# Kernel tuning notes

Hardware: AMD Instinct MI355X
Metric: run time of the kernel (lower is better)

The kernel has to match this reference:

```python
import jax, jax.numpy as jnp
import numpy as np

GAMMA = -0.1   # l0_gamma
ZETA = 1.1     # l0_zeta
BETA = 0.66    # l0_beta (hard-concrete temperature)
LAMBDA = 0.01  # lambda_reg (post-warmup current_lambda)
EPS = 1e-12


def _layernorm(x, g, b, eps=1e-5):
    mu = jnp.mean(x, axis=-1, keepdims=True)
    var = jnp.var(x, axis=-1, keepdims=True)
    return (x - mu) / jnp.sqrt(var + eps) * g + b


def setup_inputs() -> dict:
    key = jax.random.key(0)
    ks = jax.random.split(key, 12)
    B, N, D, H, E, C = 8, 512, 512, 256, 32, 2
    node_feat = jax.random.normal(ks[0], (B, N, D), jnp.float32)
    labels = jax.random.randint(ks[1], (B,), 0, C)
    a = (jax.random.uniform(ks[2], (B, N, N)) < 0.05).astype(jnp.float32)
    adjs = jnp.maximum(a, jnp.swapaxes(a, 1, 2)) * (1.0 - jnp.eye(N, dtype=jnp.float32))
    masks = jnp.ones((B, N), jnp.float32)
    init = lambda k, shp, fan: jax.random.normal(k, shp, jnp.float32) / np.sqrt(fan).astype(np.float32)
    return {
        "node_feat": node_feat, "labels": labels, "adjs": adjs, "masks": masks,
        # edge scorer MLP: concat([h_i,h_j]) -> edge_dim -> 1, factorized as Wa@h_i + Wb@h_j
        "Wa": init(ks[3], (D, E), D), "Wb": init(ks[4], (D, E), D), "be": jnp.zeros((E,), jnp.float32),
        "W2e": init(ks[5], (E, 1), E), "b2e": jnp.zeros((1,), jnp.float32),
        # conv: Linear(feature_dim, hidden_dim)
        "Wconv": init(ks[6], (D, H), D), "bconv": jnp.zeros((H,), jnp.float32),
        # classifier: Linear(H,H//2) -> ReLU -> LayerNorm -> spectral_norm(Linear(H//2,C))
        "W1c": init(ks[7], (H, H // 2), H), "b1c": jnp.zeros((H // 2,), jnp.float32),
        "ln_g": jnp.ones((H // 2,), jnp.float32), "ln_b": jnp.zeros((H // 2,), jnp.float32),
        "W2c": init(ks[8], (H // 2, C), H // 2), "b2c": jnp.zeros((C,), jnp.float32),
        "u_sn": jax.random.normal(ks[9], (C,), jnp.float32),  # spectral-norm power-iteration buffer
    }


def reference(node_feat, labels, adjs, masks, Wa, Wb, be, W2e, b2e,
              Wconv, bconv, W1c, b1c, ln_g, ln_b, W2c, b2c, u_sn):
    B = node_feat.shape[0]
    # F.normalize(node_feat, p=2, dim=2)
    nrm = jnp.sqrt(jnp.sum(node_feat * node_feat, axis=2, keepdims=True))
    nf = node_feat / jnp.maximum(nrm, EPS)
    # edge scoring: logAlpha[b,i,j] = MLP([h_i ; h_j])
    e1 = nf @ Wa                                  # [B,N,E]
    e2 = nf @ Wb                                  # [B,N,E]
    hpair = jax.nn.relu(e1[:, :, None, :] + e2[:, None, :, :] + be)   # [B,N,N,E]
    logAlpha = jnp.einsum('bije,e->bij', hpair, W2e[:, 0]) + b2e[0]    # [B,N,N]
    # deterministic hard-concrete gate (eval mode): clip(sigmoid(logAlpha)*(zeta-gamma)+gamma, 0, 1)
    gate = jnp.clip(jax.nn.sigmoid(logAlpha) * (ZETA - GAMMA) + GAMMA, 0.0, 1.0)
    edge_weights = gate * adjs
    # aggregate: row-normalized weighted adjacency
    wadj = adjs * edge_weights
    row_sum = jnp.sum(wadj, axis=2, keepdims=True) + 1e-8
    h = jnp.einsum('bij,bjd->bid', wadj / row_sum, nf)
    h = jax.nn.relu(h @ Wconv + bconv)            # [B,N,H]
    # edge-weighted attention pooling: node importance = weighted degree, masked softmax
    imp = jnp.sum(wadj, axis=2)                    # [B,N]
    attn_logits = jnp.where(masks > 0, imp, -1e9)
    attn = jax.nn.softmax(attn_logits, axis=1)
    graph_rep = jnp.einsum('bn,bnh->bh', attn, h)  # [B,H]
    # classifier
    z = jax.nn.relu(graph_rep @ W1c + b1c)
    z = _layernorm(z, ln_g, ln_b)
    # spectral norm (1 power iteration, u/v stop-gradded like torch buffers)
    v = W2c @ u_sn
    v = jax.lax.stop_gradient(v / jnp.maximum(jnp.linalg.norm(v), EPS))
    u2 = W2c.T @ v
    u2 = jax.lax.stop_gradient(u2 / jnp.maximum(jnp.linalg.norm(u2), EPS))
    sigma = v @ (W2c @ u2)
    logits = z @ (W2c / sigma) + b2c              # [B,C]
    # losses
    logp = jax.nn.log_softmax(logits, axis=1)
    cls_loss = -jnp.mean(logp[jnp.arange(B), labels])
    l0_penalty = jnp.sum(jax.nn.sigmoid(logAlpha - BETA * jnp.log(-GAMMA / ZETA)))
    total_loss = cls_loss + LAMBDA * l0_penalty
    return logits, total_loss, adjs * edge_weights
```

## Files before the change

### kernel.cpp

```cpp
#include <hip/hip_runtime.h>


#define Bsz 8
#define Nn  512
#define Dd  512
#define Hh  256
#define Ee  32

#define WS_NFCPK  0L
#define WS_E1     524288L
#define WS_E2     655360L
#define WS_WADJB  786432L
#define WS_RS     1835008L
#define WS_L0     1839104L
#define WS_GR     1839112L
#define WS_WABPK  1841160L
#define WS_WCPK   1857544L

typedef __bf16 bf16x8 __attribute__((ext_vector_type(8)));
typedef float  f32x4  __attribute__((ext_vector_type(4)));

__device__ inline ushort f2bf(float f) {
  union { float f; unsigned u; } c; c.f = f;
  return (ushort)((c.u + 0x7fffu + ((c.u >> 16) & 1u)) >> 16);
}

__global__ __launch_bounds__(256) void pack_weights(
    const float* __restrict__ Wconv, const float* __restrict__ Wa,
    const float* __restrict__ Wb, ushort* __restrict__ wcpk,
    ushort* __restrict__ wabpk)
{
  const int g = blockIdx.x*256 + threadIdx.x;
  if (g < 16384) {
    const int kq = g >> 8, n = g & 255;
    ushort tmp[8];
    #pragma unroll
    for (int j = 0; j < 8; ++j) tmp[j] = f2bf(Wconv[(kq*8 + j)*Hh + n]);
    *(uint4*)(wcpk + (long)g*8) = *(uint4*)tmp;
  } else if (g < 16384 + 4096) {
    const int gg = g - 16384;
    const int kq = gg >> 6, n = gg & 63;
    const float* W = (n < 32) ? Wa : Wb;
    const int e = n & 31;
    ushort tmp[8];
    #pragma unroll
    for (int j = 0; j < 8; ++j) tmp[j] = f2bf(W[(kq*8 + j)*Ee + e]);
    *(uint4*)(wabpk + (long)gg*8) = *(uint4*)tmp;
  }
}

__global__ __launch_bounds__(256) void norm_e12_nfc(
    const float* __restrict__ nfeat, const ushort* __restrict__ wabpk,
    const ushort* __restrict__ wcpk, const float* __restrict__ be,
    ushort* __restrict__ nfcpk, float* __restrict__ e1, float* __restrict__ e2,
    float* __restrict__ row_sum, float* __restrict__ gr,
    float* __restrict__ l0_sum)
{
  const int blk = blockIdx.x;
  const int r0 = blk*16;
  const int b = r0 >> 9;
  const int t = threadIdx.x;
  const int r = t >> 4;
  const int seg = t & 15;

  __shared__ ushort As[(63*17 + 15 + 1)*8];
  __shared__ ushort BsA[2][4*64*8];
  __shared__ ushort BsC[2][4*256*8];

  float4 v[8];
  const float* src = nfeat + (long)(r0 + r)*Dd + seg*32;
  #pragma unroll
  for (int i = 0; i < 8; ++i) v[i] = *(const float4*)(src + i*4);
  float s = 0.f;
  #pragma unroll
  for (int i = 0; i < 8; ++i)
    s += v[i].x*v[i].x + v[i].y*v[i].y + v[i].z*v[i].z + v[i].w*v[i].w;
  #pragma unroll
  for (int m = 1; m < 16; m <<= 1) s += __shfl_xor(s, m, 16);
  const float sc = 1.f / fmaxf(sqrtf(s), 1e-12f);
  #pragma unroll
  for (int q = 0; q < 4; ++q) {
    ushort tmp[8];
    const float4 a = v[2*q], bq = v[2*q+1];
    tmp[0]=f2bf(a.x*sc);  tmp[1]=f2bf(a.y*sc);  tmp[2]=f2bf(a.z*sc);  tmp[3]=f2bf(a.w*sc);
    tmp[4]=f2bf(bq.x*sc); tmp[5]=f2bf(bq.y*sc); tmp[6]=f2bf(bq.z*sc); tmp[7]=f2bf(bq.w*sc);
    *(uint4*)(As + ((seg*4 + q)*17 + r)*8) = *(uint4*)tmp;
  }
  if (t < 16) row_sum[r0 + t] = 0.f;
  if (blk == 0) {
    for (int p = t; p < Bsz*Hh; p += 256) gr[p] = 0.f;
    if (t == 0) *l0_sum = 0.f;
  }

  const int lane = t & 63, l15 = lane & 15, quad = lane >> 4;
  const int w = t >> 6;
  const int abq = t >> 6, abn = t & 63;

  f32x4 acc_e = {0.f, 0.f, 0.f, 0.f};
  f32x4 acc_c[4];
  #pragma unroll
  for (int j = 0; j < 4; ++j) acc_c[j] = (f32x4){0.f,0.f,0.f,0.f};

  uint4 pab = *(const uint4*)(wabpk + ((long)abq*64 + abn)*8);
  uint4 pc[4];
  #pragma unroll
  for (int p = 0; p < 4; ++p) {
    const int g = t + p*256;
    pc[p] = *(const uint4*)(wcpk + ((long)(g >> 8)*256 + (g & 255))*8);
  }
  *(uint4*)(BsA[0] + (abq*64 + abn)*8) = pab;
  #pragma unroll
  for (int p = 0; p < 4; ++p) {
    const int g = t + p*256;
    *(uint4*)(BsC[0] + ((g >> 8)*256 + (g & 255))*8) = pc[p];
  }
  {
    pab = *(const uint4*)(wabpk + ((long)(4 + abq)*64 + abn)*8);
    #pragma unroll
    for (int p = 0; p < 4; ++p) {
      const int g = t + p*256;
      pc[p] = *(const uint4*)(wcpk + ((long)(4 + (g >> 8))*256 + (g & 255))*8);
    }
  }

  for (int k0 = 0; k0 < 512; k0 += 32) {
    const int pb = (k0 >> 5) & 1;
    __syncthreads();
    if (k0 + 32 < 512) {
      *(uint4*)(BsA[1-pb] + (abq*64 + abn)*8) = pab;
      #pragma unroll
      for (int p = 0; p < 4; ++p) {
        const int g = t + p*256;
        *(uint4*)(BsC[1-pb] + ((g >> 8)*256 + (g & 255))*8) = pc[p];
      }
      if (k0 + 64 < 512) {
        const int kb = (k0 + 64) >> 3;
        pab = *(const uint4*)(wabpk + ((long)(kb + abq)*64 + abn)*8);
        #pragma unroll
        for (int p = 0; p < 4; ++p) {
          const int g = t + p*256;
          pc[p] = *(const uint4*)(wcpk + ((long)(kb + (g >> 8))*256 + (g & 255))*8);
        }
      }
    }
    const bf16x8 af = *(const bf16x8*)(As + (((k0 >> 3) + quad)*17 + l15)*8);
    const bf16x8 bfa = *(const bf16x8*)(BsA[pb] + (quad*64 + w*16 + l15)*8);
    acc_e = __builtin_amdgcn_mfma_f32_16x16x32_bf16(af, bfa, acc_e, 0, 0, 0);
    #pragma unroll
    for (int fn = 0; fn < 4; ++fn) {
      const bf16x8 bfc = *(const bf16x8*)(BsC[pb] + (quad*256 + w*64 + fn*16 + l15)*8);
      acc_c[fn] = __builtin_amdgcn_mfma_f32_16x16x32_bf16(af, bfc, acc_c[fn], 0, 0, 0);
    }
  }

  {
    const int col = w*16 + l15;
    #pragma unroll
    for (int rr = 0; rr < 4; ++rr) {
      const int row = r0 + quad*4 + rr;
      if (col < 32) e1[(long)row*Ee + col] = acc_e[rr] + be[col];
      else          e2[(long)row*Ee + (col - 32)] = acc_e[rr];
    }
  }

  __syncthreads();
  ushort* tile = BsC[0];
  #pragma unroll
  for (int fn = 0; fn < 4; ++fn) {
    const int col = w*64 + fn*16 + l15;
    #pragma unroll
    for (int rr = 0; rr < 4; ++rr)
      tile[(quad*4 + rr)*260 + col] = f2bf(acc_c[fn][rr]);
  }
  __syncthreads();
  #pragma unroll
  for (int p = 0; p < 2; ++p) {
    const int g = t + p*256;
    const int oct = g >> 8, c = g & 255;
    ushort tmp[8];
    #pragma unroll
    for (int j = 0; j < 8; ++j) tmp[j] = tile[(oct*8 + j)*260 + c];
    const long og = ((r0 & 511) >> 3) + oct;
    *(uint4*)(nfcpk + ((long)b*16384 + og*256 + c)*8) = *(uint4*)tmp;
  }
}

__global__ __launch_bounds__(256) void edge_kernel(
    const float* __restrict__ e1, const float* __restrict__ e2,
    const float* __restrict__ W2e, const float* __restrict__ b2e,
    const float* __restrict__ adjs, float* __restrict__ out_wadj,
    ushort* __restrict__ wadj_b, float* __restrict__ row_sum,
    float* __restrict__ l0_sum)
{
  const int b  = blockIdx.z;
  const int i0 = blockIdx.y * 32;
  const int j0 = blockIdx.x * 128;
  const int t  = threadIdx.x;

  __shared__ float e2s[32*132];

  #pragma unroll
  for (int itr = 0; itr < 4; ++itr) {
    const int idx = t + itr*256;
    const int kq = idx & 7, jg = idx >> 3;
    const float4 v = *(const float4*)(e2 + ((long)(b*Nn + j0 + jg))*Ee + kq*4);
    e2s[(kq*4+0)*132 + jg] = v.x;
    e2s[(kq*4+1)*132 + jg] = v.y;
    e2s[(kq*4+2)*132 + jg] = v.z;
    e2s[(kq*4+3)*132 + jg] = v.w;
  }

  const int pair  = t >> 4;
  const int jslot = t & 15;
  const int ia = i0 + pair*2;
  const int ib = ia + 1;
  const int ja = jslot*4;
  const int jb = ja + 64;

  float e1af[32], e1bf[32], w2f[32];
  #pragma unroll
  for (int q = 0; q < 8; ++q) {
    *(float4*)(&e1af[q*4]) = *(const float4*)(e1 + ((long)(b*Nn + ia))*Ee + q*4);
    *(float4*)(&e1bf[q*4]) = *(const float4*)(e1 + ((long)(b*Nn + ib))*Ee + q*4);
    *(float4*)(&w2f[q*4])  = *(const float4*)(W2e + q*4);
  }
  const float b2 = b2e[0];
  __syncthreads();

  float acc[2][8] = {};
  #pragma unroll
  for (int k = 0; k < 32; ++k) {
    const float4 va = *(const float4*)(e2s + k*132 + ja);
    const float4 vb = *(const float4*)(e2s + k*132 + jb);
    const float w = w2f[k];
    const float ea = e1af[k], eb = e1bf[k];
    acc[0][0] += fmaxf(ea+va.x, 0.f)*w;
    acc[0][1] += fmaxf(ea+va.y, 0.f)*w;
    acc[0][2] += fmaxf(ea+va.z, 0.f)*w;
    acc[0][3] += fmaxf(ea+va.w, 0.f)*w;
    acc[0][4] += fmaxf(ea+vb.x, 0.f)*w;
    acc[0][5] += fmaxf(ea+vb.y, 0.f)*w;
    acc[0][6] += fmaxf(ea+vb.z, 0.f)*w;
    acc[0][7] += fmaxf(ea+vb.w, 0.f)*w;
    acc[1][0] += fmaxf(eb+va.x, 0.f)*w;
    acc[1][1] += fmaxf(eb+va.y, 0.f)*w;
    acc[1][2] += fmaxf(eb+va.z, 0.f)*w;
    acc[1][3] += fmaxf(eb+va.w, 0.f)*w;
    acc[1][4] += fmaxf(eb+vb.x, 0.f)*w;
    acc[1][5] += fmaxf(eb+vb.y, 0.f)*w;
    acc[1][6] += fmaxf(eb+vb.z, 0.f)*w;
    acc[1][7] += fmaxf(eb+vb.w, 0.f)*w;
  }

  float rs[2] = {0.f, 0.f};
  float l0acc = 0.f;
  #pragma unroll
  for (int ii = 0; ii < 2; ++ii) {
    const int i = (ii == 0) ? ia : ib;
    const float* arow = adjs     + ((long)(b*Nn + i))*Nn + j0;
    ushort* bwrow     = wadj_b   + ((long)(b*Nn + i))*Nn + j0;
    float* outrow     = out_wadj + ((long)(b*Nn + i))*Nn + j0;
    #pragma unroll
    for (int h2 = 0; h2 < 2; ++h2) {
      const int jl = (h2 == 0) ? ja : jb;
      const float4 av = *(const float4*)(arow + jl);
      float wv[4];
      #pragma unroll
      for (int c = 0; c < 4; ++c) {
        const float logA = acc[ii][h2*4 + c] + b2;
        const float e = expf(-logA);
        const float sg = 1.f/(1.f + e);
        const float gate = fminf(fmaxf(sg*1.2f - 0.1f, 0.f), 1.f);
        const float a = (c==0)?av.x:(c==1)?av.y:(c==2)?av.z:av.w;
        const float w = gate*a*a;
        wv[c] = w;
        rs[ii] += w;
        l0acc += 1.f/(1.f + 0.20543832f*e);
      }
      ushort4 bw;
      bw.x = f2bf(wv[0]); bw.y = f2bf(wv[1]); bw.z = f2bf(wv[2]); bw.w = f2bf(wv[3]);
      *(ushort4*)(bwrow + jl) = bw;
      outrow[jl+0] = wv[0]; outrow[jl+1] = wv[1];
      outrow[jl+2] = wv[2]; outrow[jl+3] = wv[3];
    }
  }

  #pragma unroll
  for (int m = 1; m < 16; m <<= 1) {
    rs[0] += __shfl_xor(rs[0], m, 16);
    rs[1] += __shfl_xor(rs[1], m, 16);
  }
  if (jslot == 0) {
    atomicAdd(&row_sum[b*Nn + ia], rs[0]);
    atomicAdd(&row_sum[b*Nn + ib], rs[1]);
  }
  #pragma unroll
  for (int m = 1; m < 64; m <<= 1) l0acc += __shfl_xor(l0acc, m, 64);
  if ((t & 63) == 0) atomicAdd(l0_sum, l0acc);
}

__global__ __launch_bounds__(256) void gemm_pool(
    const ushort* __restrict__ wadjb, const ushort* __restrict__ nfcpk,
    const float* __restrict__ row_sum, const float* __restrict__ masks,
    const float* __restrict__ bconv, float* __restrict__ gr)
{
  const int bb = blockIdx.z;
  const int m0 = blockIdx.y*64, n0 = blockIdx.x*64;
  const int t = threadIdx.x;
  const int lane = t & 63, l15 = lane & 15, quad = lane >> 4;
  const int wv = t >> 6, wr = wv & 1, wc = wv >> 1;

  __shared__ ushort As[2][259*8];
  __shared__ ushort Bs[2][256*8];
  __shared__ float ptile[64*65];
  __shared__ float red[8];
  __shared__ float attn_s[64];

  const ushort* Ab = wadjb + (long)bb*262144;
  const ushort* Bb = nfcpk + (long)bb*131072;
  const int am = t >> 2, akq = t & 3;
  const int bn = t & 63, bkq = t >> 6;

  f32x4 acc[2][2];
  #pragma unroll
  for (int i = 0; i < 2; ++i)
    #pragma unroll
    for (int j = 0; j < 2; ++j) acc[i][j] = (f32x4){0.f,0.f,0.f,0.f};

  uint4 ra = *(const uint4*)(Ab + (long)(m0+am)*512 + akq*8);
  uint4 rb = *(const uint4*)(Bb + ((long)bkq*256 + n0 + bn)*8);
  *(uint4*)(As[0] + (akq*65 + am)*8) = ra;
  *(uint4*)(Bs[0] + (bkq*64 + bn)*8) = rb;
  ra = *(const uint4*)(Ab + (long)(m0+am)*512 + 32 + akq*8);
  rb = *(const uint4*)(Bb + ((long)(4 + bkq)*256 + n0 + bn)*8);

  for (int k0 = 0; k0 < 512; k0 += 32) {
    const int pb = (k0 >> 5) & 1;
    __syncthreads();
    if (k0 + 32 < 512) {
      *(uint4*)(As[1-pb] + (akq*65 + am)*8) = ra;
      *(uint4*)(Bs[1-pb] + (bkq*64 + bn)*8) = rb;
      if (k0 + 64 < 512) {
        ra = *(const uint4*)(Ab + (long)(m0+am)*512 + (k0+64) + akq*8);
        rb = *(const uint4*)(Bb + ((long)(((k0+64) >> 3) + bkq)*256 + n0 + bn)*8);
      }
    }
    bf16x8 af[2], bfr[2];
    #pragma unroll
    for (int i = 0; i < 2; ++i)
      af[i] = *(const bf16x8*)(As[pb] + (quad*65 + wr*32 + i*16 + l15)*8);
    #pragma unroll
    for (int j = 0; j < 2; ++j)
      bfr[j] = *(const bf16x8*)(Bs[pb] + (quad*64 + wc*32 + j*16 + l15)*8);
    #pragma unroll
    for (int i = 0; i < 2; ++i)
      #pragma unroll
      for (int j = 0; j < 2; ++j)
        acc[i][j] = __builtin_amdgcn_mfma_f32_16x16x32_bf16(
            af[i], bfr[j], acc[i][j], 0, 0, 0);
  }
  __syncthreads();

  {
    const float mk0 = masks[bb*Nn + t], mk1 = masks[bb*Nn + t + 256];
    const float lv0 = (mk0 > 0.f) ? row_sum[bb*Nn + t] : -1e9f;
    const float lv1 = (mk1 > 0.f) ? row_sum[bb*Nn + t + 256] : -1e9f;
    float m = fmaxf(lv0, lv1);
    #pragma unroll
    for (int s = 1; s < 64; s <<= 1) m = fmaxf(m, __shfl_xor(m, s, 64));
    if (lane == 0) red[wv] = m;
    __syncthreads();
    const float mx = fmaxf(fmaxf(red[0], red[1]), fmaxf(red[2], red[3]));
    float sm = expf(lv0 - mx) + expf(lv1 - mx);
    #pragma unroll
    for (int s = 1; s < 64; s <<= 1) sm += __shfl_xor(sm, s, 64);
    if (lane == 0) red[4 + wv] = sm;
    __syncthreads();
    const float sinv = 1.f/(red[4] + red[5] + red[6] + red[7]);
    if (t < 64) {
      const int node = m0 + t;
      const float mm = masks[bb*Nn + node];
      const float lv = (mm > 0.f) ? row_sum[bb*Nn + node] : -1e9f;
      attn_s[t] = expf(lv - mx)*sinv;
    }
    __syncthreads();
  }

  #pragma unroll
  for (int i = 0; i < 2; ++i) {
    #pragma unroll
    for (int j = 0; j < 2; ++j) {
      const int lcol = wc*32 + j*16 + l15;
      const float bias = bconv[n0 + lcol];
      #pragma unroll
      for (int rr = 0; rr < 4; ++rr) {
        const int lrow = wr*32 + i*16 + quad*4 + rr;
        const int row = m0 + lrow;
        const float scl = 1.f/(row_sum[bb*Nn + row] + 1e-8f);
        const float hv = fmaxf(acc[i][j][rr]*scl + bias, 0.f);
        ptile[lrow*65 + lcol] = hv * attn_s[lrow];
      }
    }
  }
  __syncthreads();
  if (t < 64) {
    float s = 0.f;
    #pragma unroll 4
    for (int rr = 0; rr < 64; ++rr) s += ptile[rr*65 + t];
    atomicAdd(&gr[bb*Hh + n0 + t], s);
  }
}

__global__ __launch_bounds__(256) void classifier_kernel(
    const float* __restrict__ gr, const float* __restrict__ W1c,
    const float* __restrict__ b1c, const float* __restrict__ ln_g,
    const float* __restrict__ ln_b, const float* __restrict__ W2c,
    const float* __restrict__ b2c, const float* __restrict__ u_sn,
    const int* __restrict__ labels, const float* __restrict__ l0_sum,
    float* __restrict__ out)
{
  const int t = threadIdx.x;
  const int og = t & 31;
  const int dr = t >> 5;

  __shared__ float grs[2048];
  __shared__ float part[8][8][128];
  __shared__ float z[8][128];
  __shared__ float mu_s[8], ri_s[8];
  __shared__ float snpart[6];
  __shared__ float sinv_s;
  __shared__ float lg[16];

  float4 w[32];
  const float* wp = W1c + (long)dr*32*128 + og*4;
  #pragma unroll
  for (int i = 0; i < 32; ++i) w[i] = *(const float4*)(wp + i*128);

  #pragma unroll
  for (int p = 0; p < 8; ++p) grs[t + p*256] = gr[t + p*256];
  __syncthreads();

  float4 acc[8];
  #pragma unroll
  for (int b = 0; b < 8; ++b) acc[b] = (float4){0.f,0.f,0.f,0.f};
  #pragma unroll
  for (int i = 0; i < 32; ++i) {
    const int d = dr*32 + i;
    #pragma unroll
    for (int b = 0; b < 8; ++b) {
      const float g = grs[b*256 + d];
      acc[b].x += g*w[i].x; acc[b].y += g*w[i].y;
      acc[b].z += g*w[i].z; acc[b].w += g*w[i].w;
    }
  }
  #pragma unroll
  for (int b = 0; b < 8; ++b)
    *(float4*)(&part[dr][b][og*4]) = acc[b];
  __syncthreads();

  #pragma unroll
  for (int p = 0; p < 4; ++p) {
    const int idx = t + p*256;
    const int b = idx >> 7, o = idx & 127;
    float s = b1c[o];
    #pragma unroll
    for (int d2 = 0; d2 < 8; ++d2) s += part[d2][b][o];
    z[b][o] = fmaxf(s, 0.f);
  }
  __syncthreads();

  {
    const int b = t >> 5, g = t & 31;
    const float4 zv = *(const float4*)(&z[b][g*4]);
    float s1 = zv.x + zv.y + zv.z + zv.w;
    #pragma unroll
    for (int m = 1; m < 32; m <<= 1) s1 += __shfl_xor(s1, m, 32);
    const float mu = s1*(1.f/128.f);
    float s2 = (zv.x-mu)*(zv.x-mu) + (zv.y-mu)*(zv.y-mu)
             + (zv.z-mu)*(zv.z-mu) + (zv.w-mu)*(zv.w-mu);
    #pragma unroll
    for (int m = 1; m < 32; m <<= 1) s2 += __shfl_xor(s2, m, 32);
    if (g == 0) { mu_s[b] = mu; ri_s[b] = rsqrtf(s2*(1.f/128.f) + 1e-5f); }
  }

  if (t < 128) {
    const float w0 = W2c[2*t], w1 = W2c[2*t+1];
    const float vt = w0*u_sn[0] + w1*u_sn[1];
    float svv = vt*vt, sa = vt*w0, sb = vt*w1;
    #pragma unroll
    for (int m = 1; m < 64; m <<= 1) {
      svv += __shfl_xor(svv, m, 64);
      sa  += __shfl_xor(sa , m, 64);
      sb  += __shfl_xor(sb , m, 64);
    }
    if ((t & 63) == 0) {
      const int wd = t >> 6;
      snpart[wd*3+0] = svv; snpart[wd*3+1] = sa; snpart[wd*3+2] = sb;
    }
  }
  __syncthreads();
  if (t == 0) {
    const float svv = snpart[0] + snpart[3];
    const float sa  = snpart[1] + snpart[4];
    const float sb  = snpart[2] + snpart[5];
    const float vninv = 1.f/fmaxf(sqrtf(svv), 1e-12f);
    const float u20 = sa*vninv, u21 = sb*vninv;
    const float uninv = 1.f/fmaxf(sqrtf(u20*u20 + u21*u21), 1e-12f);
    const float u2n0 = u20*uninv, u2n1 = u21*uninv;
    const float sigma = vninv*(u2n0*sa + u2n1*sb);
    sinv_s = 1.f/sigma;
  }
  __syncthreads();

  {
    const float sinv = sinv_s;
    const int grp = t >> 4, g = t & 15;
    const int b = grp >> 1, c = grp & 1;
    const float mu = mu_s[b], ri = ri_s[b];
    float acc2 = 0.f;
    #pragma unroll
    for (int j = 0; j < 8; ++j) {
      const int o = g*8 + j;
      const float zln = (z[b][o]-mu)*ri*ln_g[o] + ln_b[o];
      acc2 += zln*W2c[2*o + c];
    }
    #pragma unroll
    for (int m = 1; m < 16; m <<= 1) acc2 += __shfl_xor(acc2, m, 16);
    if (g == 0) {
      const float lgv = acc2*sinv + b2c[c];
      lg[grp] = lgv;
      out[grp] = lgv;
    }
  }
  __syncthreads();
  if (t == 0) {
    float closs = 0.f;
    #pragma unroll
    for (int b = 0; b < 8; ++b) {
      const float a0 = lg[2*b], a1 = lg[2*b+1];
      const float m = fmaxf(a0, a1);
      const float lse = m + logf(expf(a0-m) + expf(a1-m));
      closs += lse - lg[2*b + labels[b]];
    }
    out[16] = closs*(1.f/8.f) + 0.01f*l0_sum[0];
  }
}

extern "C" void kernel_launch(void* const* d_in, const int* in_sizes, int n_in,
                              void* d_out, int out_size, void* d_ws, size_t ws_size,
                              hipStream_t stream) {
  const float* node_feat = (const float*)d_in[0];
  const int*   labels    = (const int*)d_in[1];
  const float* adjs      = (const float*)d_in[2];
  const float* masks     = (const float*)d_in[3];
  const float* Wa        = (const float*)d_in[4];
  const float* Wb        = (const float*)d_in[5];
  const float* be        = (const float*)d_in[6];
  const float* W2e       = (const float*)d_in[7];
  const float* b2e       = (const float*)d_in[8];
  const float* Wconv     = (const float*)d_in[9];
  const float* bconv     = (const float*)d_in[10];
  const float* W1c       = (const float*)d_in[11];
  const float* b1c       = (const float*)d_in[12];
  const float* ln_g      = (const float*)d_in[13];
  const float* ln_b      = (const float*)d_in[14];
  const float* W2c       = (const float*)d_in[15];
  const float* b2c       = (const float*)d_in[16];
  const float* u_sn      = (const float*)d_in[17];

  float* out = (float*)d_out;
  float* ws  = (float*)d_ws;
  ushort* nfcpk  = (ushort*)(ws + WS_NFCPK);
  float*  e1     = ws + WS_E1;
  float*  e2     = ws + WS_E2;
  ushort* wadjb  = (ushort*)(ws + WS_WADJB);
  float*  row_sum= ws + WS_RS;
  float*  l0s    = ws + WS_L0;
  float*  gr     = ws + WS_GR;
  ushort* wabpk  = (ushort*)(ws + WS_WABPK);
  ushort* wcpk   = (ushort*)(ws + WS_WCPK);

  pack_weights<<<80, 256, 0, stream>>>(Wconv, Wa, Wb, wcpk, wabpk);
  norm_e12_nfc<<<256, 256, 0, stream>>>(node_feat, wabpk, wcpk, be, nfcpk,
                                        e1, e2, row_sum, gr, l0s);
  edge_kernel<<<dim3(Nn/128, Nn/32, Bsz), 256, 0, stream>>>(
      e1, e2, W2e, b2e, adjs, out + 17, wadjb, row_sum, l0s);
  gemm_pool<<<dim3(Hh/64, Nn/64, Bsz), 256, 0, stream>>>(
      wadjb, nfcpk, row_sum, masks, bconv, gr);
  classifier_kernel<<<1, 256, 0, stream>>>(gr, W1c, b1c, ln_g, ln_b, W2c, b2c,
                                           u_sn, labels, l0s, out);
}
```

Measured before the change: 174.9 us.

## Shrink edge_kernel tiles and replace global L0 atomic with per-block partials

The edge kernel tile shrinks from 32x128 to 16x64 per block, giving each thread one row and four columns. This launches four times more blocks (2048) to fill the GPU better, at the cost of lower per-thread reuse of e2 data from shared memory. The single global atomicAdd for the L0 penalty becomes per-block partial sums in workspace, which the classifier kernel reduces. That removes atomic contention and the need to zero the accumulator.

```diff
diff --git a/kernel.cpp b/kernel.cpp
--- a/kernel.cpp
+++ b/kernel.cpp
@@ -16,6 +16,7 @@
 #define WS_GR     1839112L
 #define WS_WABPK  1841160L
 #define WS_WCPK   1857544L
+#define WS_L0P    1923080L
 
 typedef __bf16 bf16x8 __attribute__((ext_vector_type(8)));
 typedef float  f32x4  __attribute__((ext_vector_type(4)));
@@ -53,8 +54,7 @@
     const float* __restrict__ nfeat, const ushort* __restrict__ wabpk,
     const ushort* __restrict__ wcpk, const float* __restrict__ be,
     ushort* __restrict__ nfcpk, float* __restrict__ e1, float* __restrict__ e2,
-    float* __restrict__ row_sum, float* __restrict__ gr,
-    float* __restrict__ l0_sum)
+    float* __restrict__ row_sum, float* __restrict__ gr)
 {
   const int blk = blockIdx.x;
   const int r0 = blk*16;
@@ -89,7 +89,6 @@
   if (t < 16) row_sum[r0 + t] = 0.f;
   if (blk == 0) {
     for (int p = t; p < Bsz*Hh; p += 256) gr[p] = 0.f;
-    if (t == 0) *l0_sum = 0.f;
   }
 
   const int lane = t & 63, l15 = lane & 15, quad = lane >> 4;
@@ -190,113 +189,89 @@
     const float* __restrict__ W2e, const float* __restrict__ b2e,
     const float* __restrict__ adjs, float* __restrict__ out_wadj,
     ushort* __restrict__ wadj_b, float* __restrict__ row_sum,
-    float* __restrict__ l0_sum)
+    float* __restrict__ l0_part)
 {
   const int b  = blockIdx.z;
-  const int i0 = blockIdx.y * 32;
-  const int j0 = blockIdx.x * 128;
+  const int i0 = blockIdx.y * 16;
+  const int j0 = blockIdx.x * 64;
   const int t  = threadIdx.x;
 
-  __shared__ float e2s[32*132];
-
-  #pragma unroll
-  for (int itr = 0; itr < 4; ++itr) {
+  __shared__ float e2s[32*68];
+  __shared__ float l0red[4];
+
+  #pragma unroll
+  for (int itr = 0; itr < 2; ++itr) {
     const int idx = t + itr*256;
     const int kq = idx & 7, jg = idx >> 3;
     const float4 v = *(const float4*)(e2 + ((long)(b*Nn + j0 + jg))*Ee + kq*4);
-    e2s[(kq*4+0)*132 + jg] = v.x;
-    e2s[(kq*4+1)*132 + jg] = v.y;
-    e2s[(kq*4+2)*132 + jg] = v.z;
-    e2s[(kq*4+3)*132 + jg] = v.w;
-  }
-
-  const int pair  = t >> 4;
+    e2s[(kq*4+0)*68 + jg] = v.x;
+    e2s[(kq*4+1)*68 + jg] = v.y;
+    e2s[(kq*4+2)*68 + jg] = v.z;
+    e2s[(kq*4+3)*68 + jg] = v.w;
+  }
+
+  const int row   = t >> 4;
   const int jslot = t & 15;
-  const int ia = i0 + pair*2;
-  const int ib = ia + 1;
-  const int ja = jslot*4;
-  const int jb = ja + 64;
-
-  float e1af[32], e1bf[32], w2f[32];
+  const int i  = i0 + row;
+  const int jl = jslot*4;
+
+  const float4 av = *(const float4*)(adjs + ((long)(b*Nn + i))*Nn + j0 + jl);
+
+  float e1f[32], w2f[32];
   #pragma unroll
   for (int q = 0; q < 8; ++q) {
-    *(float4*)(&e1af[q*4]) = *(const float4*)(e1 + ((long)(b*Nn + ia))*Ee + q*4);
-    *(float4*)(&e1bf[q*4]) = *(const float4*)(e1 + ((long)(b*Nn + ib))*Ee + q*4);
-    *(float4*)(&w2f[q*4])  = *(const float4*)(W2e + q*4);
+    *(float4*)(&e1f[q*4]) = *(const float4*)(e1 + ((long)(b*Nn + i))*Ee + q*4);
+    *(float4*)(&w2f[q*4]) = *(const float4*)(W2e + q*4);
   }
   const float b2 = b2e[0];
   __syncthreads();
 
-  float acc[2][8] = {};
+  float acc[4] = {0.f, 0.f, 0.f, 0.f};
   #pragma unroll
   for (int k = 0; k < 32; ++k) {
-    const float4 va = *(const float4*)(e2s + k*132 + ja);
-    const float4 vb = *(const float4*)(e2s + k*132 + jb);
+    const float4 va = *(const float4*)(e2s + k*68 + jl);
     const float w = w2f[k];
-    const float ea = e1af[k], eb = e1bf[k];
-    acc[0][0] += fmaxf(ea+va.x, 0.f)*w;
-    acc[0][1] += fmaxf(ea+va.y, 0.f)*w;
-    acc[0][2] += fmaxf(ea+va.z, 0.f)*w;
-    acc[0][3] += fmaxf(ea+va.w, 0.f)*w;
-    acc[0][4] += fmaxf(ea+vb.x, 0.f)*w;
-    acc[0][5] += fmaxf(ea+vb.y, 0.f)*w;
-    acc[0][6] += fmaxf(ea+vb.z, 0.f)*w;
-    acc[0][7] += fmaxf(ea+vb.w, 0.f)*w;
-    acc[1][0] += fmaxf(eb+va.x, 0.f)*w;
-    acc[1][1] += fmaxf(eb+va.y, 0.f)*w;
-    acc[1][2] += fmaxf(eb+va.z, 0.f)*w;
-    acc[1][3] += fmaxf(eb+va.w, 0.f)*w;
-    acc[1][4] += fmaxf(eb+vb.x, 0.f)*w;
-    acc[1][5] += fmaxf(eb+vb.y, 0.f)*w;
-    acc[1][6] += fmaxf(eb+vb.z, 0.f)*w;
-    acc[1][7] += fmaxf(eb+vb.w, 0.f)*w;
-  }
-
-  float rs[2] = {0.f, 0.f};
-  float l0acc = 0.f;
-  #pragma unroll
-  for (int ii = 0; ii < 2; ++ii) {
-    const int i = (ii == 0) ? ia : ib;
-    const float* arow = adjs     + ((long)(b*Nn + i))*Nn + j0;
-    ushort* bwrow     = wadj_b   + ((long)(b*Nn + i))*Nn + j0;
-    float* outrow     = out_wadj + ((long)(b*Nn + i))*Nn + j0;
-    #pragma unroll
-    for (int h2 = 0; h2 < 2; ++h2) {
-      const int jl = (h2 == 0) ? ja : jb;
-      const float4 av = *(const float4*)(arow + jl);
-      float wv[4];
-      #pragma unroll
-      for (int c = 0; c < 4; ++c) {
-        const float logA = acc[ii][h2*4 + c] + b2;
-        const float e = expf(-logA);
-        const float sg = 1.f/(1.f + e);
-        const float gate = fminf(fmaxf(sg*1.2f - 0.1f, 0.f), 1.f);
-        const float a = (c==0)?av.x:(c==1)?av.y:(c==2)?av.z:av.w;
-        const float w = gate*a*a;
-        wv[c] = w;
-        rs[ii] += w;
-        l0acc += 1.f/(1.f + 0.20543832f*e);
-      }
-      ushort4 bw;
-      bw.x = f2bf(wv[0]); bw.y = f2bf(wv[1]); bw.z = f2bf(wv[2]); bw.w = f2bf(wv[3]);
-      *(ushort4*)(bwrow + jl) = bw;
-      outrow[jl+0] = wv[0]; outrow[jl+1] = wv[1];
-      outrow[jl+2] = wv[2]; outrow[jl+3] = wv[3];
-    }
-  }
-
-  #pragma unroll
-  for (int m = 1; m < 16; m <<= 1) {
-    rs[0] += __shfl_xor(rs[0], m, 16);
-    rs[1] += __shfl_xor(rs[1], m, 16);
-  }
-  if (jslot == 0) {
-    atomicAdd(&row_sum[b*Nn + ia], rs[0]);
-    atomicAdd(&row_sum[b*Nn + ib], rs[1]);
-  }
+    const float ea = e1f[k];
+    acc[0] += fmaxf(ea+va.x, 0.f)*w;
+    acc[1] += fmaxf(ea+va.y, 0.f)*w;
+    acc[2] += fmaxf(ea+va.z, 0.f)*w;
+    acc[3] += fmaxf(ea+va.w, 0.f)*w;
+  }
+
+  float rs = 0.f, l0acc = 0.f;
+  float wv[4];
+  #pragma unroll
+  for (int c = 0; c < 4; ++c) {
+    const float logA = acc[c] + b2;
+    const float e = expf(-logA);
+    const float sg = 1.f/(1.f + e);
+    const float gate = fminf(fmaxf(sg*1.2f - 0.1f, 0.f), 1.f);
+    const float a = (c==0)?av.x:(c==1)?av.y:(c==2)?av.z:av.w;
+    const float w = gate*a*a;
+    wv[c] = w;
+    rs += w;
+    l0acc += 1.f/(1.f + 0.20543832f*e);
+  }
+  {
+    ushort4 bw;
+    bw.x = f2bf(wv[0]); bw.y = f2bf(wv[1]); bw.z = f2bf(wv[2]); bw.w = f2bf(wv[3]);
+    *(ushort4*)(wadj_b + ((long)(b*Nn + i))*Nn + j0 + jl) = bw;
+    float* outrow = out_wadj + ((long)(b*Nn + i))*Nn + j0 + jl;
+    outrow[0] = wv[0]; outrow[1] = wv[1];
+    outrow[2] = wv[2]; outrow[3] = wv[3];
+  }
+
+  #pragma unroll
+  for (int m = 1; m < 16; m <<= 1) rs += __shfl_xor(rs, m, 16);
+  if (jslot == 0) atomicAdd(&row_sum[b*Nn + i], rs);
+
   #pragma unroll
   for (int m = 1; m < 64; m <<= 1) l0acc += __shfl_xor(l0acc, m, 64);
-  if ((t & 63) == 0) atomicAdd(l0_sum, l0acc);
+  if ((t & 63) == 0) l0red[t >> 6] = l0acc;
+  __syncthreads();
+  if (t == 0)
+    l0_part[((long)blockIdx.z*32 + blockIdx.y)*8 + blockIdx.x] =
+        l0red[0] + l0red[1] + l0red[2] + l0red[3];
 }
 
 __global__ __launch_bounds__(256) void gemm_pool(
@@ -416,7 +391,7 @@
     const float* __restrict__ b1c, const float* __restrict__ ln_g,
     const float* __restrict__ ln_b, const float* __restrict__ W2c,
     const float* __restrict__ b2c, const float* __restrict__ u_sn,
-    const int* __restrict__ labels, const float* __restrict__ l0_sum,
+    const int* __restrict__ labels, const float* __restrict__ l0_part,
     float* __restrict__ out)
 {
   const int t = threadIdx.x;
@@ -428,6 +403,7 @@
   __shared__ float z[8][128];
   __shared__ float mu_s[8], ri_s[8];
   __shared__ float snpart[6];
+  __shared__ float l0w[4];
   __shared__ float sinv_s;
   __shared__ float lg[16];
 
@@ -438,6 +414,12 @@
 
   #pragma unroll
   for (int p = 0; p < 8; ++p) grs[t + p*256] = gr[t + p*256];
+  float l0t = 0.f;
+  #pragma unroll
+  for (int p = 0; p < 8; ++p) l0t += l0_part[t + p*256];
+  #pragma unroll
+  for (int m = 1; m < 64; m <<= 1) l0t += __shfl_xor(l0t, m, 64);
+  if ((t & 63) == 0) l0w[t >> 6] = l0t;
   __syncthreads();
 
   float4 acc[8];
@@ -542,7 +524,8 @@
       const float lse = m + logf(expf(a0-m) + expf(a1-m));
       closs += lse - lg[2*b + labels[b]];
     }
-    out[16] = closs*(1.f/8.f) + 0.01f*l0_sum[0];
+    const float l0 = l0w[0] + l0w[1] + l0w[2] + l0w[3];
+    out[16] = closs*(1.f/8.f) + 0.01f*l0;
   }
 }
 
@@ -575,18 +558,18 @@
   float*  e2     = ws + WS_E2;
   ushort* wadjb  = (ushort*)(ws + WS_WADJB);
   float*  row_sum= ws + WS_RS;
-  float*  l0s    = ws + WS_L0;
   float*  gr     = ws + WS_GR;
   ushort* wabpk  = (ushort*)(ws + WS_WABPK);
   ushort* wcpk   = (ushort*)(ws + WS_WCPK);
+  float*  l0p    = ws + WS_L0P;
 
   pack_weights<<<80, 256, 0, stream>>>(Wconv, Wa, Wb, wcpk, wabpk);
   norm_e12_nfc<<<256, 256, 0, stream>>>(node_feat, wabpk, wcpk, be, nfcpk,
-                                        e1, e2, row_sum, gr, l0s);
-  edge_kernel<<<dim3(Nn/128, Nn/32, Bsz), 256, 0, stream>>>(
-      e1, e2, W2e, b2e, adjs, out + 17, wadjb, row_sum, l0s);
+                                        e1, e2, row_sum, gr);
+  edge_kernel<<<dim3(Nn/64, Nn/16, Bsz), 256, 0, stream>>>(
+      e1, e2, W2e, b2e, adjs, out + 17, wadjb, row_sum, l0p);
   gemm_pool<<<dim3(Hh/64, Nn/64, Bsz), 256, 0, stream>>>(
       wadjb, nfcpk, row_sum, masks, bconv, gr);
   classifier_kernel<<<1, 256, 0, stream>>>(gr, W1c, b1c, ln_g, ln_b, W2c, b2c,
-                                           u_sn, labels, l0s, out);
-}
+                                           u_sn, labels, l0p, out);
+}
```

New measurement: 165.0 us. 5.7% less time.
